# Performance work log

Measured on AMD Instinct MI355X. Metric: run time of the kernel, lower is better.

The kernel has to match this reference:

```python
import math
import jax, jax.numpy as jnp
import numpy as np

N_HEAD = 16
DIM = 1024
HEAD_DIM = DIM // N_HEAD  # 64


def _rope(x):
    # x: [b, h, t, d] ; lucidrains RotaryEmbedding default: interleaved pairs,
    # inv_freq = 1/theta^(2i/d), theta=10000, positions = arange(t)
    t, d = x.shape[2], x.shape[3]
    inv_freq = 1.0 / (10000.0 ** (jnp.arange(0, d, 2, dtype=jnp.float32) / d))  # [d/2]
    freqs = jnp.arange(t, dtype=jnp.float32)[:, None] * inv_freq[None, :]       # [t, d/2]
    emb = jnp.repeat(freqs, 2, axis=-1)                                          # [t, d]
    cos = jnp.cos(emb).astype(x.dtype)
    sin = jnp.sin(emb).astype(x.dtype)
    x1 = x[..., ::2]
    x2 = x[..., 1::2]
    rot = jnp.stack([-x2, x1], axis=-1).reshape(x.shape)  # rotate_half (interleaved)
    return x * cos + rot * sin


def setup_inputs() -> dict:
    key = jax.random.key(0)
    k1, k2, k3 = jax.random.split(key, 3)
    b, t = 2, 2048
    x = jax.random.normal(k1, (b, t, DIM), dtype=jnp.float32)
    w_qkv = jax.random.normal(k2, (DIM, 3 * DIM), dtype=jnp.float32) * (1.0 / math.sqrt(DIM))
    b_qkv = jnp.zeros((3 * DIM,), dtype=jnp.float32)
    w_out = jax.random.normal(k3, (DIM, DIM), dtype=jnp.float32) * (1.0 / math.sqrt(DIM))
    b_out = jnp.zeros((DIM,), dtype=jnp.float32)
    return {"x": x, "w_qkv": w_qkv, "b_qkv": b_qkv, "w_out": w_out, "b_out": b_out}


def reference(x, w_qkv, b_qkv, w_out, b_out):
    b, t, d = x.shape
    qkv = jnp.einsum('btd,de->bte', x, w_qkv) + b_qkv  # [b,t,3d]
    q, k, v = jnp.split(qkv, 3, axis=-1)
    # [b,t,d] -> [b,h,t,nd]
    def heads(z):
        return z.reshape(b, t, N_HEAD, HEAD_DIM).transpose(0, 2, 1, 3)
    q, k, v = heads(q), heads(k), heads(v)
    q = _rope(q)
    k = _rope(k)
    attn = jnp.einsum('bhqd,bhkd->bhqk', q, k) / math.sqrt(HEAD_DIM)
    attn = jax.nn.softmax(attn, axis=-1)
    # dropout is identity in eval mode
    out = jnp.einsum('bhqk,bhkd->bhqd', attn, v)
    out = out.transpose(0, 2, 1, 3).reshape(b, t, d)
    return jnp.einsum('btd,de->bte', out, w_out) + b_out
```

## Files before the change

kernel.cpp:

```cpp
#include <hip/hip_runtime.h>
#include <hip/hip_bf16.h>

typedef unsigned short u16;
typedef unsigned int u32;
typedef __attribute__((ext_vector_type(8))) short bf16x8;
typedef __attribute__((ext_vector_type(4))) float f32x4;
typedef __attribute__((ext_vector_type(16))) float f32x16;

typedef __attribute__((address_space(1))) const u32* gas_ptr;
typedef __attribute__((address_space(3))) u32* las_ptr;

__device__ __forceinline__ void gld16(const void* g, void* l) {
  __builtin_amdgcn_global_load_lds((gas_ptr)g, (las_ptr)l, 16, 0, 0);
}

__device__ __forceinline__ u16 f2bf(float f) {
  unsigned u = __float_as_uint(f);
  u = u + 0x7fffu + ((u >> 16) & 1u);
  return (u16)(u >> 16);
}

__global__ __launch_bounds__(256) void prep(const float* __restrict__ x, u16* __restrict__ x_bf,
                                            const float* __restrict__ wqkv, u16* __restrict__ wqkvT,
                                            const float* __restrict__ wout, u16* __restrict__ woutT,
                                            float2* __restrict__ cs) {
  __shared__ float tile[32][33];
  const int b = blockIdx.x, tid = threadIdx.x;
  if (b < 4096) {
    int i = b * 256 + tid;
    float4 v = reinterpret_cast<const float4*>(x)[i];
    ushort4 o = make_ushort4(f2bf(v.x), f2bf(v.y), f2bf(v.z), f2bf(v.w));
    reinterpret_cast<ushort4*>(x_bf)[i] = o;
  } else if (b < 8192) {
    const float* in; u16* out; int R, C, bx, by;
    if (b < 7168) { in = wqkv; out = wqkvT; R = 1024; C = 3072; int b2 = b - 4096; bx = b2 % 96; by = b2 / 96; }
    else          { in = wout; out = woutT; R = 1024; C = 1024; int b3 = b - 7168; bx = b3 % 32; by = b3 / 32; }
    int tx = tid & 31, ty = tid >> 5;
    int c0 = bx * 32, r0 = by * 32;
#pragma unroll
    for (int i = 0; i < 32; i += 8)
      tile[ty + i][tx] = in[(size_t)(r0 + ty + i) * C + c0 + tx];
    __syncthreads();
#pragma unroll
    for (int i = 0; i < 32; i += 8)
      out[(size_t)(c0 + ty + i) * R + r0 + tx] = f2bf(tile[tx][ty + i]);
  } else {
    int idx = (b - 8192) * 256 + tid;
    int i = idx & 31, t = idx >> 5;
    float invf = powf(10000.0f, -(float)(2 * i) / 64.0f);
    float f = (float)t * invf;
    cs[idx] = make_float2(cosf(f), sinf(f));
  }
}

#define BKK 32
template <int BNT, int MODE>
__global__ __launch_bounds__(256) void gemm_bt(
    const u16* __restrict__ A, const u16* __restrict__ Bt, const float* __restrict__ bias,
    float* __restrict__ Cf, u16* __restrict__ q_ws, u16* __restrict__ k_ws, u16* __restrict__ v_ws,
    const float2* __restrict__ cs, int M, int N, int K) {
  constexpr int NJ = BNT / 32;
  __shared__ u16 As[128][BKK];
  __shared__ u16 Bs[BNT][BKK];
  const int tid = threadIdx.x;
  const int lane = tid & 63;
  const int wid = tid >> 6;
  const int wr = wid >> 1, wc = wid & 1;
  const int fr = lane & 15, fg = lane >> 4;
  const int m0 = blockIdx.y * 128, n0 = blockIdx.x * BNT;

  const int row_l = lane >> 2;
  const int slot_l = lane & 3;

  f32x4 acc[4][NJ] = {};

  for (int k0 = 0; k0 < K; k0 += BKK) {
#pragma unroll
    for (int i = 0; i < 2; i++) {
      int rowA = wid * 32 + i * 16;
      gld16(A + (size_t)(m0 + rowA + row_l) * K + k0 + slot_l * 8, &As[rowA][0]);
    }
#pragma unroll
    for (int i = 0; i < BNT / 64; i++) {
      int rowB = wid * (BNT / 4) + i * 16;
      gld16(Bt + (size_t)(n0 + rowB + row_l) * K + k0 + slot_l * 8, &Bs[rowB][0]);
    }
    __syncthreads();
    bf16x8 af[4], bfr[NJ];
#pragma unroll
    for (int i = 0; i < 4; i++)
      af[i] = *reinterpret_cast<const bf16x8*>(&As[wr * 64 + i * 16 + fr][fg * 8]);
#pragma unroll
    for (int j = 0; j < NJ; j++)
      bfr[j] = *reinterpret_cast<const bf16x8*>(&Bs[wc * (BNT / 2) + j * 16 + fr][fg * 8]);
#pragma unroll
    for (int i = 0; i < 4; i++)
#pragma unroll
      for (int j = 0; j < NJ; j++)
        acc[i][j] = __builtin_amdgcn_mfma_f32_16x16x32_bf16(af[i], bfr[j], acc[i][j], 0, 0, 0);
    __syncthreads();
  }

#pragma unroll
  for (int i = 0; i < 4; i++) {
    int rowb = m0 + wr * 64 + i * 16 + fg * 4;
#pragma unroll
    for (int j = 0; j < NJ; j++) {
      int col = n0 + wc * (BNT / 2) + j * 16 + fr;
      float bv = bias[col];
      if (MODE == 0) {
#pragma unroll
        for (int r = 0; r < 4; r++)
          Cf[(size_t)(rowb + r) * N + col] = acc[i][j][r] + bv;
      } else {
        int bb = rowb >> 11, t0 = rowb & 2047;
        int sec = col >> 10, nn = col & 1023;
        int h = nn >> 6, d = nn & 63;
        int bh = (bb << 4) + h;
        if (sec == 2) {
          ushort4 st;
          st.x = f2bf(acc[i][j][0] + bv);
          st.y = f2bf(acc[i][j][1] + bv);
          st.z = f2bf(acc[i][j][2] + bv);
          st.w = f2bf(acc[i][j][3] + bv);
          *reinterpret_cast<ushort4*>(v_ws + ((size_t)(bh * 64 + d)) * 2048 + t0) = st;
        } else {
          u16* dst = (sec == 0) ? q_ws : k_ws;
#pragma unroll
          for (int r = 0; r < 4; r++) {
            float v = acc[i][j][r] + bv;
            float vp = __shfl_xor(v, 1);
            int t = t0 + r;
            float2 c_s = cs[(t << 5) + (d >> 1)];
            float vv = (d & 1) ? fmaf(v, c_s.x, vp * c_s.y) : fmaf(v, c_s.x, -vp * c_s.y);
            dst[((size_t)bh * 2048 + t) * 64 + d] = f2bf(vv);
          }
        }
      }
    }
  }
}

#define KVB 64
#define NT 32
#define CSC 0.18033688011112042f
#define MSUB 11.5415603f

__global__ __launch_bounds__(256, 2) void attn_fwd(const u16* __restrict__ q_ws,
                                                   const u16* __restrict__ k_ws,
                                                   const u16* __restrict__ v_ws,
                                                   u16* __restrict__ attn_out) {
  __shared__ u16 Klds[2][4096];
  __shared__ u16 Vlds[2][4096];

  const int tid = threadIdx.x, lane = tid & 63, w = tid >> 6;
  const int l31 = lane & 31, hi = lane >> 5;
  const int bid = blockIdx.x;
  const int wrk = (bid & 7) * 64 + (bid >> 3);
  const int bh = wrk >> 4;
  const int q0 = (wrk & 15) * 128 + w * 32;
  const size_t base = (size_t)bh * (2048 * 64);

  bf16x8 qf[4];
#pragma unroll
  for (int db = 0; db < 4; db++)
    qf[db] = *reinterpret_cast<const bf16x8*>(
        q_ws + base + (size_t)(q0 + l31) * 64 + db * 16 + hi * 8);

  bf16x8 onesv;
#pragma unroll
  for (int i = 0; i < 8; i++) onesv[i] = (short)0x3F80;

  f32x16 Oa[2] = {};
  f32x16 l_acc = {};

  const int krow_l = lane >> 3, kslot_l = lane & 7;
  const u16* kg = k_ws + base;
  const u16* vgT = v_ws + base;

#define STAGE_K(kv, buf)                                                          \
  {                                                                               \
    _Pragma("unroll") for (int i = 0; i < 2; i++) {                               \
      int row = w * 16 + i * 8 + krow_l;                                          \
      int srcslot = kslot_l ^ (row & 7);                                          \
      gld16(kg + (size_t)((kv) + row) * 64 + srcslot * 8, &Klds[buf][(w * 16 + i * 8) * 64]); \
    }                                                                             \
  }
#define STAGE_V(kv, buf)                                                          \
  {                                                                               \
    _Pragma("unroll") for (int i = 0; i < 2; i++) {                               \
      int row = w * 16 + i * 8 + krow_l;                             \
      int srcslot = kslot_l ^ (row & 7);                                          \
      gld16(vgT + (size_t)row * 2048 + (kv) + srcslot * 8, &Vlds[buf][(w * 16 + i * 8) * 64]); \
    }                                                                             \
  }

  STAGE_K(0, 0);
  STAGE_V(0, 0);
  __syncthreads();

  int cur = 0;
  for (int t = 0; t < NT; t++) {
    if (t + 1 < NT) {
      STAGE_K((t + 1) * KVB, cur ^ 1);
      STAGE_V((t + 1) * KVB, cur ^ 1);
    }

    const char* Kb = (const char*)&Klds[cur][0];
    const char* Vb = (const char*)&Vlds[cur][0];

    bf16x8 kf[2][4];
#pragma unroll
    for (int ks = 0; ks < 2; ks++) {
      int krow = (l31 + 32 * ks) * 128;
      int ksw = (l31 & 7) << 4;
#pragma unroll
      for (int db = 0; db < 4; db++)
        kf[ks][db] = *reinterpret_cast<const bf16x8*>(Kb + krow + ((db * 32 + hi * 16) ^ ksw));
    }

    f32x16 s0 = {}, s1 = {};
    __builtin_amdgcn_s_setprio(1);
#pragma unroll
    for (int db = 0; db < 4; db++) {
      s0 = __builtin_amdgcn_mfma_f32_32x32x16_bf16(kf[0][db], qf[db], s0, 0, 0, 0);
      s1 = __builtin_amdgcn_mfma_f32_32x32x16_bf16(kf[1][db], qf[db], s1, 0, 0, 0);
    }
    __builtin_amdgcn_s_setprio(0);

    float p[32];
#pragma unroll
    for (int i = 0; i < 16; i++) {
      p[i]      = exp2f(fmaf(s0[i], CSC, -MSUB));
      p[16 + i] = exp2f(fmaf(s1[i], CSC, -MSUB));
    }

    union U4 { u32 u[4]; bf16x8 v; };
    U4 pf[4];
#pragma unroll
    for (int kk = 0; kk < 2; kk++)
#pragma unroll
      for (int wd = 0; wd < 8; wd++) {
        __hip_bfloat162 hh =
            __float22bfloat162_rn(make_float2(p[kk * 16 + 2 * wd], p[kk * 16 + 2 * wd + 1]));
        u32 uu;
        __builtin_memcpy(&uu, &hh, 4);
        pf[kk * 2 + (wd >> 2)].u[wd & 3] = uu;
      }

    __builtin_amdgcn_s_setprio(1);
#pragma unroll
    for (int kb = 0; kb < 4; kb++)
      l_acc = __builtin_amdgcn_mfma_f32_32x32x16_bf16(onesv, pf[kb].v, l_acc, 0, 0, 0);

    int vsw = (l31 & 7) << 4;
#pragma unroll
    for (int ds = 0; ds < 2; ds++) {
      int vrow = (l31 + 32 * ds) * 128;
#pragma unroll
      for (int kb = 0; kb < 4; kb++) {
        uint2 va = *(const uint2*)(Vb + vrow + ((kb * 32 + hi * 8) ^ vsw));
        uint2 vb2 = *(const uint2*)(Vb + vrow + ((kb * 32 + hi * 8 + 16) ^ vsw));
        U4 vf;
        vf.u[0] = va.x; vf.u[1] = va.y; vf.u[2] = vb2.x; vf.u[3] = vb2.y;
        Oa[ds] = __builtin_amdgcn_mfma_f32_32x32x16_bf16(vf.v, pf[kb].v, Oa[ds], 0, 0, 0);
      }
    }
    __builtin_amdgcn_s_setprio(0);

    __syncthreads();
    cur ^= 1;
  }

  const int b = bh >> 4, h = bh & 15;
  float invl = 1.0f / l_acc[0];
  int row = q0 + l31;
  size_t rbase = ((size_t)(b * 2048 + row)) * 1024 + h * 64;
#pragma unroll
  for (int ds = 0; ds < 2; ds++)
#pragma unroll
    for (int rg = 0; rg < 4; rg++) {
      int d0 = rg * 8 + hi * 4 + ds * 32;
      ushort4 st;
      st.x = f2bf(Oa[ds][rg * 4 + 0] * invl);
      st.y = f2bf(Oa[ds][rg * 4 + 1] * invl);
      st.z = f2bf(Oa[ds][rg * 4 + 2] * invl);
      st.w = f2bf(Oa[ds][rg * 4 + 3] * invl);
      *reinterpret_cast<ushort4*>(attn_out + rbase + d0) = st;
    }
#undef STAGE_K
#undef STAGE_V
}

extern "C" void kernel_launch(void* const* d_in, const int* in_sizes, int n_in,
                              void* d_out, int out_size, void* d_ws, size_t ws_size,
                              hipStream_t stream) {
  const float* x     = (const float*)d_in[0];
  const float* w_qkv = (const float*)d_in[1];
  const float* b_qkv = (const float*)d_in[2];
  const float* w_out = (const float*)d_in[3];
  const float* b_out = (const float*)d_in[4];
  float* out = (float*)d_out;

  char* ws = (char*)d_ws;
  const size_t MB = 1024 * 1024;
  u16*    x_bf   = (u16*)(ws);
  u16*    wqkvT  = (u16*)(ws + 8 * MB);
  u16*    woutT  = (u16*)(ws + 14 * MB);
  u16*    q_ws   = (u16*)(ws + 16 * MB);
  u16*    k_ws   = (u16*)(ws + 24 * MB);
  u16*    v_ws   = (u16*)(ws + 32 * MB);
  u16*    attn_o = (u16*)(ws + 40 * MB);
  float2* cs     = (float2*)(ws + 48 * MB);

  prep<<<8448, 256, 0, stream>>>(x, x_bf, w_qkv, wqkvT, w_out, woutT, cs);
  gemm_bt<128, 1><<<dim3(24, 32), 256, 0, stream>>>(x_bf, wqkvT, b_qkv, nullptr,
                                                    q_ws, k_ws, v_ws, cs, 4096, 3072, 1024);
  attn_fwd<<<512, 256, 0, stream>>>(q_ws, k_ws, v_ws, attn_o);
  gemm_bt<64, 0><<<dim3(16, 32), 256, 0, stream>>>(attn_o, woutT, b_out, out,
                                                   nullptr, nullptr, nullptr, nullptr,
                                                   4096, 1024, 1024);
}
```

Before: 232.3 us.

## Double GEMM K-tile with swizzled LDS and replace MFMA row-sum with VALU reduction

The GEMM K-tile grows from 32 to 64 with an XOR-swizzled LDS layout, so each barrier pair covers twice the MFMA work and the wider rows avoid bank conflicts. It also adds an occupancy hint to launch_bounds. In attention, the softmax denominator is no longer computed with extra MFMAs against a ones vector; it is summed per lane in fp32 and combined across half-waves with a shuffle at the end. V fragment loads are hoisted ahead of the PV MFMA batch. The costs are more LDS and registers per GEMM block, and denominators summed from unrounded fp32 values where the PV product uses bf16-rounded P.

```diff
diff --git a/kernel.cpp b/kernel.cpp
--- a/kernel.cpp
+++ b/kernel.cpp
@@ -53,9 +53,9 @@
   }
 }
 
-#define BKK 32
+#define BKK 64
 template <int BNT, int MODE>
-__global__ __launch_bounds__(256) void gemm_bt(
+__global__ __launch_bounds__(256, 3) void gemm_bt(
     const u16* __restrict__ A, const u16* __restrict__ Bt, const float* __restrict__ bias,
     float* __restrict__ Cf, u16* __restrict__ q_ws, u16* __restrict__ k_ws, u16* __restrict__ v_ws,
     const float2* __restrict__ cs, int M, int N, int K) {
@@ -69,35 +69,49 @@
   const int fr = lane & 15, fg = lane >> 4;
   const int m0 = blockIdx.y * 128, n0 = blockIdx.x * BNT;
 
-  const int row_l = lane >> 2;
-  const int slot_l = lane & 3;
+  const int row_l = lane >> 3;
+  const int slot_l = lane & 7;
+  const int srcoff = (slot_l ^ row_l) * 8;
 
   f32x4 acc[4][NJ] = {};
 
   for (int k0 = 0; k0 < K; k0 += BKK) {
 #pragma unroll
-    for (int i = 0; i < 2; i++) {
-      int rowA = wid * 32 + i * 16;
-      gld16(A + (size_t)(m0 + rowA + row_l) * K + k0 + slot_l * 8, &As[rowA][0]);
-    }
-#pragma unroll
-    for (int i = 0; i < BNT / 64; i++) {
-      int rowB = wid * (BNT / 4) + i * 16;
-      gld16(Bt + (size_t)(n0 + rowB + row_l) * K + k0 + slot_l * 8, &Bs[rowB][0]);
+    for (int i = 0; i < 4; i++) {
+      int r8 = wid * 32 + i * 8;
+      gld16(A + (size_t)(m0 + r8 + row_l) * K + k0 + srcoff, &As[r8][0]);
+    }
+#pragma unroll
+    for (int i = 0; i < BNT / 32; i++) {
+      int r8 = wid * (BNT / 4) + i * 8;
+      gld16(Bt + (size_t)(n0 + r8 + row_l) * K + k0 + srcoff, &Bs[r8][0]);
     }
     __syncthreads();
-    bf16x8 af[4], bfr[NJ];
+    bf16x8 af[4][2], bfr[NJ][2];
+    const char* Ab = (const char*)&As[0][0];
+    const char* Bb = (const char*)&Bs[0][0];
+    int fsw = (fr & 7) << 4;
+#pragma unroll
+    for (int i = 0; i < 4; i++) {
+      int row = wr * 64 + i * 16 + fr;
+#pragma unroll
+      for (int ks = 0; ks < 2; ks++)
+        af[i][ks] = *reinterpret_cast<const bf16x8*>(Ab + row * 128 + ((ks * 64 + fg * 16) ^ fsw));
+    }
+#pragma unroll
+    for (int j = 0; j < NJ; j++) {
+      int row = wc * (BNT / 2) + j * 16 + fr;
+#pragma unroll
+      for (int ks = 0; ks < 2; ks++)
+        bfr[j][ks] = *reinterpret_cast<const bf16x8*>(Bb + row * 128 + ((ks * 64 + fg * 16) ^ fsw));
+    }
 #pragma unroll
     for (int i = 0; i < 4; i++)
-      af[i] = *reinterpret_cast<const bf16x8*>(&As[wr * 64 + i * 16 + fr][fg * 8]);
-#pragma unroll
-    for (int j = 0; j < NJ; j++)
-      bfr[j] = *reinterpret_cast<const bf16x8*>(&Bs[wc * (BNT / 2) + j * 16 + fr][fg * 8]);
-#pragma unroll
-    for (int i = 0; i < 4; i++)
 #pragma unroll
       for (int j = 0; j < NJ; j++)
-        acc[i][j] = __builtin_amdgcn_mfma_f32_16x16x32_bf16(af[i], bfr[j], acc[i][j], 0, 0, 0);
+#pragma unroll
+        for (int ks = 0; ks < 2; ks++)
+          acc[i][j] = __builtin_amdgcn_mfma_f32_16x16x32_bf16(af[i][ks], bfr[j][ks], acc[i][j], 0, 0, 0);
     __syncthreads();
   }
 
@@ -167,12 +181,8 @@
     qf[db] = *reinterpret_cast<const bf16x8*>(
         q_ws + base + (size_t)(q0 + l31) * 64 + db * 16 + hi * 8);
 
-  bf16x8 onesv;
-#pragma unroll
-  for (int i = 0; i < 8; i++) onesv[i] = (short)0x3F80;
-
   f32x16 Oa[2] = {};
-  f32x16 l_acc = {};
+  float l_lane = 0.f;
 
   const int krow_l = lane >> 3, kslot_l = lane & 7;
   const u16* kg = k_ws + base;
@@ -235,6 +245,18 @@
       p[16 + i] = exp2f(fmaf(s1[i], CSC, -MSUB));
     }
 
+    {
+      float q0s = (p[0] + p[1]) + (p[2] + p[3]);
+      float q1s = (p[4] + p[5]) + (p[6] + p[7]);
+      float q2s = (p[8] + p[9]) + (p[10] + p[11]);
+      float q3s = (p[12] + p[13]) + (p[14] + p[15]);
+      float q4s = (p[16] + p[17]) + (p[18] + p[19]);
+      float q5s = (p[20] + p[21]) + (p[22] + p[23]);
+      float q6s = (p[24] + p[25]) + (p[26] + p[27]);
+      float q7s = (p[28] + p[29]) + (p[30] + p[31]);
+      l_lane += ((q0s + q1s) + (q2s + q3s)) + ((q4s + q5s) + (q6s + q7s));
+    }
+
     union U4 { u32 u[4]; bf16x8 v; };
     U4 pf[4];
 #pragma unroll
@@ -248,12 +270,8 @@
         pf[kk * 2 + (wd >> 2)].u[wd & 3] = uu;
       }
 
-    __builtin_amdgcn_s_setprio(1);
-#pragma unroll
-    for (int kb = 0; kb < 4; kb++)
-      l_acc = __builtin_amdgcn_mfma_f32_32x32x16_bf16(onesv, pf[kb].v, l_acc, 0, 0, 0);
-
     int vsw = (l31 & 7) << 4;
+    U4 vf[2][4];
 #pragma unroll
     for (int ds = 0; ds < 2; ds++) {
       int vrow = (l31 + 32 * ds) * 128;
@@ -261,11 +279,16 @@
       for (int kb = 0; kb < 4; kb++) {
         uint2 va = *(const uint2*)(Vb + vrow + ((kb * 32 + hi * 8) ^ vsw));
         uint2 vb2 = *(const uint2*)(Vb + vrow + ((kb * 32 + hi * 8 + 16) ^ vsw));
-        U4 vf;
-        vf.u[0] = va.x; vf.u[1] = va.y; vf.u[2] = vb2.x; vf.u[3] = vb2.y;
-        Oa[ds] = __builtin_amdgcn_mfma_f32_32x32x16_bf16(vf.v, pf[kb].v, Oa[ds], 0, 0, 0);
+        vf[ds][kb].u[0] = va.x; vf[ds][kb].u[1] = va.y;
+        vf[ds][kb].u[2] = vb2.x; vf[ds][kb].u[3] = vb2.y;
       }
     }
+    __builtin_amdgcn_s_setprio(1);
+#pragma unroll
+    for (int ds = 0; ds < 2; ds++)
+#pragma unroll
+      for (int kb = 0; kb < 4; kb++)
+        Oa[ds] = __builtin_amdgcn_mfma_f32_32x32x16_bf16(vf[ds][kb].v, pf[kb].v, Oa[ds], 0, 0, 0);
     __builtin_amdgcn_s_setprio(0);
 
     __syncthreads();
@@ -273,7 +296,8 @@
   }
 
   const int b = bh >> 4, h = bh & 15;
-  float invl = 1.0f / l_acc[0];
+  float l = l_lane + __shfl_xor(l_lane, 32);
+  float invl = 1.0f / l;
   int row = q0 + l31;
   size_t rbase = ((size_t)(b * 2048 + row)) * 1024 + h * 64;
 #pragma unroll
```

Result: faster. 208.8 us (-10.1%).
